# Kernel optimization log

Hardware: AMD Instinct MI355X
Metric: run time of the kernel (lower is better)

The kernel has to match this reference:

```python
import jax, jax.numpy as jnp
import numpy as np

H, KVH, HD, E, TOPK = 16, 4, 128, 8, 2
EPS = 1.1920929e-07  # fp32 machine eps, matches F.rms_norm default


def _rms(v):
    return v * jax.lax.rsqrt(jnp.mean(jnp.square(v), axis=-1, keepdims=True) + EPS)


def _rope(t, cos, sin):
    d = t.shape[-1] // 2
    t1, t2 = t[..., :d], t[..., d:]
    return jnp.concatenate([t1 * cos + t2 * sin, -t1 * sin + t2 * cos], axis=-1)


def setup_inputs():
    key = jax.random.key(0)
    ks = jax.random.split(key, 10)
    B, T, C, D = 2, 1024, 2048, 512
    # real rotary tables (broadcast over batch and heads)
    inv = 1.0 / (10000.0 ** (np.arange(HD // 2, dtype=np.float64) / (HD // 2)))
    ang = np.arange(T, dtype=np.float64)[:, None] * inv[None, :]
    cos = jnp.asarray(np.cos(ang), jnp.float32)[None, :, None, :]
    sin = jnp.asarray(np.sin(ang), jnp.float32)[None, :, None, :]
    w = lambda k, shp, fan: jax.random.normal(k, shp, jnp.float32) * (fan ** -0.5)
    return {
        'x': jax.random.normal(ks[0], (B, T, C), jnp.float32),
        'cos': cos, 'sin': sin,
        'Wq': w(ks[1], (C, C), C),
        'Wk': w(ks[2], (C, KVH * HD), C),
        'Wv': w(ks[3], (C, KVH * HD), C),
        'Wo': w(ks[4], (C, C), C),
        'Wr': w(ks[5], (C, E), C),
        'Ws1': w(ks[6], (C, D), C),
        'Ws2': w(ks[7], (D, C), D),
        'We1': w(ks[8], (E, C, D), C),
        'We2': w(ks[9], (E, D, C), D),
    }


def reference(x, cos, sin, Wq, Wk, Wv, Wo, Wr, Ws1, Ws2, We1, We2):
    B, T, C = x.shape
    # ---- attention (pre-norm, RoPE, QK-norm, GQA, causal SDPA) ----
    xn = _rms(x)
    q = _rms(_rope((xn @ Wq).reshape(B, T, H, HD), cos, sin))      # [B,T,H,HD]
    k = _rms(_rope((xn @ Wk).reshape(B, T, KVH, HD), cos, sin))    # [B,T,KVH,HD]
    v = (xn @ Wv).reshape(B, T, KVH, HD)
    rep = H // KVH
    k = jnp.repeat(k, rep, axis=2)
    v = jnp.repeat(v, rep, axis=2)
    scores = jnp.einsum('bthd,bshd->bhts', q, k) / np.float32(np.sqrt(HD))
    causal = jnp.tril(jnp.ones((T, T), bool))
    scores = jnp.where(causal, scores, jnp.float32(-np.inf))
    att = jax.nn.softmax(scores, axis=-1)
    y = jnp.einsum('bhts,bshd->bthd', att, v).reshape(B, T, C) @ Wo
    x = x + y
    # ---- DeepSeekMoE (shared expert + top-k routed experts) ----
    xf = _rms(x).reshape(-1, C)                                    # [N,C]
    N = xf.shape[0]
    shared = jnp.square(jax.nn.relu(xf @ Ws1)) @ Ws2               # [N,C]
    logits = xf @ Wr                                               # [N,E]
    tk_w, tk_idx = jax.lax.top_k(logits, TOPK)
    tk_w = jax.nn.softmax(tk_w.astype(jnp.float32), axis=-1).astype(x.dtype)
    # scatter top-k probs into dense per-expert gates (indices unique per row)
    gates = jnp.zeros((N, E), x.dtype).at[jnp.arange(N)[:, None], tk_idx].set(tk_w)
    h = jnp.square(jax.nn.relu(jnp.einsum('nc,ecd->end', xf, We1)))  # [E,N,D]
    routed = jnp.einsum('end,edc,ne->nc', h, We2, gates)             # [N,C]
    return x + (shared + routed).reshape(B, T, C)
```

## Files before the change

### kernel.cpp

```cpp
#include <hip/hip_runtime.h>

typedef _Float16 h16;
typedef _Float16 half8 __attribute__((ext_vector_type(8)));
typedef float f32x4 __attribute__((ext_vector_type(4)));

#define EPS_RMS 1.1920929e-07f
#define MiB (1ull << 20)

__device__ __forceinline__ void gload_lds16(const void* g, void* l) {
  __builtin_amdgcn_global_load_lds(
      (const __attribute__((address_space(1))) unsigned int*)g,
      (__attribute__((address_space(3))) unsigned int*)l, 16, 0, 0);
}

struct GemmP {
  const h16* Ah; const h16* Al;
  const h16* Bh; const h16* Bl;
  float* Cf; h16* Ch; h16* Cl;
  const float* R;
  const int* cnt; const int* off; const int* perm;
  long sAz, sBz, sCzHi, sCzLo;
  int M, N, K, lda, ldb, ldc;
  int zAoff, zBoff, zCoff, bzShift, czHiShift, czLoMask;
  float outScale;
};

template <int SPLIT, int EPI, int USECNT, int GATHER, int ASYNC>
__global__ __launch_bounds__(256, 4) void gemm_k(GemmP p) {
  constexpr int NP = SPLIT ? 2 : 1;
  constexpr int NBUF = (ASYNC == 1) ? 2 : 1;
  constexpr int APAD = (ASYNC == 1) ? 32 : 40;
  constexpr int BPAD = (ASYNC >= 1) ? 32 : 40;
  __shared__ __align__(16) h16 As[NBUF][NP][128][APAD];
  __shared__ __align__(16) h16 Bs[NBUF][NP][128][BPAD];
  __shared__ int permLds[GATHER ? 128 : 1];

  int bm, bn, zl;
  if constexpr (USECNT) {
    const int flat2d = blockIdx.y * gridDim.x + blockIdx.x;
    zl = flat2d & 7;
    const int idx = (flat2d >> 3) * 8 + blockIdx.z;
    bm = idx % gridDim.x;
    bn = idx / gridDim.x;
  } else {
    const int nwg = gridDim.x * gridDim.y;
    const int flat = blockIdx.y * gridDim.x + blockIdx.x;
    const int q8 = nwg >> 3, r8 = nwg & 7;
    const int xcd = flat & 7, sub = flat >> 3;
    const int swz = (xcd < r8 ? xcd * (q8 + 1) : r8 * (q8 + 1) + (xcd - r8) * q8) + sub;
    bm = swz % gridDim.x;
    bn = swz / gridDim.x;
    zl = blockIdx.z;
  }

  int Meff, rowbase;
  if (USECNT) {
    Meff = p.cnt[zl]; rowbase = p.off[zl];
    if (bm * 128 >= Meff) return;
  } else { Meff = p.M; rowbase = 0; }

  const int zA = zl + p.zAoff, zB = zl + p.zBoff, zC = zl + p.zCoff;
  const h16* Ah = p.Ah + (size_t)zA * p.sAz;
  const h16* Al = SPLIT ? p.Al + (size_t)zA * p.sAz : (const h16*)0;
  const size_t bofs = (size_t)(zB >> p.bzShift) * p.sBz;
  const h16* Bh = p.Bh + bofs;
  const h16* Bl = SPLIT ? p.Bl + bofs : (const h16*)0;
  const size_t cofs = (size_t)(zC >> p.czHiShift) * p.sCzHi +
                      (size_t)(zC & p.czLoMask) * p.sCzLo;

  const int tid = threadIdx.x;
  const int lane = tid & 63;
  const int wid = tid >> 6, wr = wid >> 1, wc = wid & 1;
  const int fr = lane & 15, fq = lane >> 4;

  if (GATHER) {
    if (tid < 128) {
      const int local = bm * 128 + tid;
      permLds[tid] = (local < Meff) ? p.perm[rowbase + local] : -1;
    }
    __syncthreads();
  }

  const long arow0 = (long)rowbase + (long)bm * 128;

  const f32x4 fz = {0.f, 0.f, 0.f, 0.f};
  f32x4 acc[4][4];
#pragma unroll
  for (int m = 0; m < 4; ++m)
#pragma unroll
    for (int n = 0; n < 4; ++n) acc[m][n] = fz;

  const int nkt = p.K / 32;

  auto compute = [&](int buf) {
    half8 af[NP][4], bf[NP][4];
#pragma unroll
    for (int m = 0; m < 4; ++m) {
      const int r = wr * 64 + m * 16 + fr;
      af[0][m] = *(const half8*)&As[buf][0][r][fq * 8];
      if (SPLIT) af[1][m] = *(const half8*)&As[buf][1][r][fq * 8];
    }
#pragma unroll
    for (int n = 0; n < 4; ++n) {
      const int c = wc * 64 + n * 16 + fr;
      bf[0][n] = *(const half8*)&Bs[buf][0][c][fq * 8];
      if (SPLIT) bf[1][n] = *(const half8*)&Bs[buf][1][c][fq * 8];
    }
#pragma unroll
    for (int m = 0; m < 4; ++m)
#pragma unroll
      for (int n = 0; n < 4; ++n) {
        acc[m][n] = __builtin_amdgcn_mfma_f32_16x16x32_f16(af[0][m], bf[0][n], acc[m][n], 0, 0, 0);
        if (SPLIT) {
          acc[m][n] = __builtin_amdgcn_mfma_f32_16x16x32_f16(af[0][m], bf[1][n], acc[m][n], 0, 0, 0);
          acc[m][n] = __builtin_amdgcn_mfma_f32_16x16x32_f16(af[1][m], bf[0][n], acc[m][n], 0, 0, 0);
        }
      }
  };

  if constexpr (ASYNC == 1) {
    auto stage = [&](int buf, int kt) {
      const int kb = kt * 32;
#pragma unroll
      for (int it = 0; it < 2; ++it) {
        const int d = (tid + it * 256) * 16;
        const int row = d >> 6;
        const int oct = (d >> 4) & 3;
        const size_t gb = ((size_t)(bn * 128 + row)) * p.ldb + kb + oct * 8;
        gload_lds16(Bh + gb, (char*)&Bs[buf][0][0][0] + d);
        if (SPLIT) gload_lds16(Bl + gb, (char*)&Bs[buf][1][0][0] + d);
        const size_t ga = (size_t)(arow0 + row) * p.lda + kb + oct * 8;
        gload_lds16(Ah + ga, (char*)&As[buf][0][0][0] + d);
        if (SPLIT) gload_lds16(Al + ga, (char*)&As[buf][1][0][0] + d);
      }
    };
    stage(0, 0);
    __syncthreads();
    int cur = 0;
    for (int kt = 0; kt < nkt; ++kt) {
      if (kt + 1 < nkt) stage(cur ^ 1, kt + 1);
      compute(cur);
      __syncthreads();
      cur ^= 1;
    }
  } else {
    for (int kt = 0; kt < nkt; ++kt) {
      if (kt) __syncthreads();
      const int kb = kt * 32;
      if constexpr (ASYNC == 2) {
#pragma unroll
        for (int it = 0; it < 2; ++it) {
          const int d = (tid + it * 256) * 16;
          const int row = d >> 6;
          const int oct = (d >> 4) & 3;
          const size_t gb = ((size_t)(bn * 128 + row)) * p.ldb + kb + oct * 8;
          gload_lds16(Bh + gb, (char*)&Bs[0][0][0][0] + d);
          if (SPLIT) gload_lds16(Bl + gb, (char*)&Bs[0][1][0][0] + d);
        }
      }
#pragma unroll
      for (int s = 0; s < 2; ++s) {
        const int seg = tid * 2 + s;
        const int row = seg >> 2, ks = (seg & 3) * 8;
        const int local = bm * 128 + row;
        bool av; long arow;
        if (GATHER) { const int tk2 = permLds[row]; av = (tk2 >= 0); arow = tk2; }
        else { av = (local < Meff); arow = (long)rowbase + local; }
        half8 vh = {0,0,0,0,0,0,0,0}, vl = {0,0,0,0,0,0,0,0};
        if (av) {
          vh = *(const half8*)(Ah + arow * (size_t)p.lda + kb + ks);
          if (SPLIT) vl = *(const half8*)(Al + arow * (size_t)p.lda + kb + ks);
        }
        *(half8*)&As[0][0][row][ks] = vh;
        if (SPLIT) *(half8*)&As[0][1][row][ks] = vl;
        if constexpr (ASYNC == 0) {
          const long brow = (long)bn * 128 + row;
          *(half8*)&Bs[0][0][row][ks] = *(const half8*)(Bh + brow * (size_t)p.ldb + kb + ks);
          if (SPLIT)
            *(half8*)&Bs[0][1][row][ks] = *(const half8*)(Bl + brow * (size_t)p.ldb + kb + ks);
        }
      }
      __syncthreads();
      compute(0);
    }
  }

#pragma unroll
  for (int m = 0; m < 4; ++m)
#pragma unroll
    for (int n = 0; n < 4; ++n)
#pragma unroll
      for (int j = 0; j < 4; ++j) {
        const int rl = wr * 64 + m * 16 + fq * 4 + j;
        const int cl = wc * 64 + n * 16 + fr;
        const int local = bm * 128 + rl;
        if (local >= Meff) continue;
        const size_t idx = cofs + ((size_t)rowbase + local) * p.ldc + (size_t)bn * 128 + cl;
        const float v = acc[m][n][j] * p.outScale;
        if (EPI == 0) p.Cf[idx] = v;
        else if (EPI == 1) p.Cf[idx] = v + p.R[idx];
        else if (EPI == 2) {
          const h16 hh = (h16)v;
          p.Ch[idx] = hh; p.Cl[idx] = (h16)(v - (float)hh);
        } else if (EPI == 3) {
          const float r2 = v > 0.f ? v * v : 0.f;
          p.Ch[idx] = (h16)r2;
        } else {
          p.Ch[idx] = (h16)v;
        }
      }
}

__global__ __launch_bounds__(512, 1) void flash_k(
    const h16* __restrict__ Qh, const h16* __restrict__ Ql,
    const h16* __restrict__ Kh, const h16* __restrict__ Kl,
    const h16* __restrict__ Vh, const h16* __restrict__ Vl,
    h16* __restrict__ yh, h16* __restrict__ yl,
    float* __restrict__ yp, float* __restrict__ mp, float* __restrict__ lp) {
  __shared__ __align__(16) h16 Ks[2][32][136];
  __shared__ __align__(16) h16 Vs[2][128][40];
  __shared__ __align__(16) h16 Ps[8][2][16][40];

  const int item = blockIdx.x, z = blockIdx.y;
  int qb, chunk;
  if (item < 4) { qb = item; chunk = 0; }
  else { qb = 4 + ((item - 4) >> 1); chunk = (item - 4) & 1; }
  const int nt = (qb + 1) * 4;
  const int tBeg = (item < 4) ? 0 : (chunk ? nt / 2 : 0);
  const int tEnd = (item < 4) ? nt : (chunk ? nt : nt / 2);

  const int b = z >> 4, h = z & 15;
  const size_t qoff = (size_t)z * 131072;
  const size_t koff = (size_t)(b * 4 + (h >> 2)) * 131072;

  const int tid = threadIdx.x;
  const int lane = tid & 63, w = tid >> 6;
  const int fr = lane & 15, fq = lane >> 4;

  const int qrow = qb * 128 + w * 16 + fr;
  half8 qa[2][4];
#pragma unroll
  for (int kt = 0; kt < 4; ++kt) {
    qa[0][kt] = *(const half8*)(Qh + qoff + (size_t)qrow * 128 + kt * 32 + fq * 8);
    qa[1][kt] = *(const half8*)(Ql + qoff + (size_t)qrow * 128 + kt * 32 + fq * 8);
  }

  const int kRow = tid >> 4, kSeg = tid & 15;
  const int vRow = tid >> 2, vSeg = tid & 3;

  const f32x4 fz = {0.f, 0.f, 0.f, 0.f};
  f32x4 y[8];
#pragma unroll
  for (int n = 0; n < 8; ++n) y[n] = fz;
  float mrow[4] = {-3.0e38f, -3.0e38f, -3.0e38f, -3.0e38f};
  float lrow[4] = {0.f, 0.f, 0.f, 0.f};

  for (int t = tBeg; t < tEnd; ++t) {
    const int kvb = t * 32;
    if (t != tBeg) __syncthreads();
#pragma unroll
    for (int pl = 0; pl < 2; ++pl) {
      const h16* kp = pl ? Kl : Kh;
      const h16* vp = pl ? Vl : Vh;
      *(half8*)&Ks[pl][kRow][kSeg * 8] =
          *(const half8*)(kp + koff + (size_t)(kvb + kRow) * 128 + kSeg * 8);
      *(half8*)&Vs[pl][vRow][vSeg * 8] =
          *(const half8*)(vp + koff + (size_t)vRow * 1024 + kvb + vSeg * 8);
    }
    __syncthreads();

    f32x4 sf[2] = {fz, fz};
#pragma unroll
    for (int n = 0; n < 2; ++n)
#pragma unroll
      for (int kt = 0; kt < 4; ++kt) {
        const half8 bh2 = *(const half8*)&Ks[0][n * 16 + fr][kt * 32 + fq * 8];
        const half8 bl2 = *(const half8*)&Ks[1][n * 16 + fr][kt * 32 + fq * 8];
        sf[n] = __builtin_amdgcn_mfma_f32_16x16x32_f16(qa[0][kt], bh2, sf[n], 0, 0, 0);
        sf[n] = __builtin_amdgcn_mfma_f32_16x16x32_f16(qa[0][kt], bl2, sf[n], 0, 0, 0);
        sf[n] = __builtin_amdgcn_mfma_f32_16x16x32_f16(qa[1][kt], bh2, sf[n], 0, 0, 0);
      }

    if (kvb + 31 > qb * 128) {
#pragma unroll
      for (int n = 0; n < 2; ++n)
#pragma unroll
        for (int j = 0; j < 4; ++j) {
          const int kvg = kvb + n * 16 + fr;
          const int qg = qb * 128 + w * 16 + fq * 4 + j;
          if (kvg > qg) sf[n][j] = -3.0e38f;
        }
    }

    float al[4];
#pragma unroll
    for (int j = 0; j < 4; ++j) {
      float tm = fmaxf(sf[0][j], sf[1][j]);
#pragma unroll
      for (int msk = 1; msk < 16; msk <<= 1) tm = fmaxf(tm, __shfl_xor(tm, msk, 16));
      const float mn = fmaxf(mrow[j], tm);
      al[j] = __expf(mrow[j] - mn);
      mrow[j] = mn;
      sf[0][j] = __expf(sf[0][j] - mn);
      sf[1][j] = __expf(sf[1][j] - mn);
      float ts = sf[0][j] + sf[1][j];
#pragma unroll
      for (int msk = 1; msk < 16; msk <<= 1) ts += __shfl_xor(ts, msk, 16);
      lrow[j] = lrow[j] * al[j] + ts;
    }
#pragma unroll
    for (int n = 0; n < 8; ++n)
#pragma unroll
      for (int j = 0; j < 4; ++j) y[n][j] *= al[j];

#pragma unroll
    for (int n = 0; n < 2; ++n)
#pragma unroll
      for (int j = 0; j < 4; ++j) {
        const float pp = sf[n][j] * 1024.f;
        const h16 hh = (h16)pp;
        Ps[w][0][fq * 4 + j][n * 16 + fr] = hh;
        Ps[w][1][fq * 4 + j][n * 16 + fr] = (h16)(pp - (float)hh);
      }

    const half8 pah = *(const half8*)&Ps[w][0][fr][fq * 8];
    const half8 pal = *(const half8*)&Ps[w][1][fr][fq * 8];
#pragma unroll
    for (int n = 0; n < 8; ++n) {
      const half8 vh2 = *(const half8*)&Vs[0][n * 16 + fr][fq * 8];
      const half8 vl2 = *(const half8*)&Vs[1][n * 16 + fr][fq * 8];
      y[n] = __builtin_amdgcn_mfma_f32_16x16x32_f16(pah, vh2, y[n], 0, 0, 0);
      y[n] = __builtin_amdgcn_mfma_f32_16x16x32_f16(pah, vl2, y[n], 0, 0, 0);
      y[n] = __builtin_amdgcn_mfma_f32_16x16x32_f16(pal, vh2, y[n], 0, 0, 0);
    }
  }

  if (item < 4) {
#pragma unroll
    for (int n = 0; n < 8; ++n)
#pragma unroll
      for (int j = 0; j < 4; ++j) {
        const int row = qb * 128 + w * 16 + fq * 4 + j;
        const int col = h * 128 + n * 16 + fr;
        const float v = y[n][j] / (1024.f * lrow[j]);
        const size_t idx = ((size_t)(b * 1024 + row)) * 2048 + col;
        const h16 hh = (h16)v;
        yh[idx] = hh; yl[idx] = (h16)(v - (float)hh);
      }
  } else {
#pragma unroll
    for (int j = 0; j < 4; ++j) {
      const int qrl = w * 16 + fq * 4 + j;
      const int q512 = (qb - 4) * 128 + qrl;
      const size_t rbase = (((size_t)chunk * 32 + z) * 512 + q512);
#pragma unroll
      for (int n = 0; n < 8; ++n)
        yp[rbase * 128 + n * 16 + fr] = y[n][j];
      if (fr == 0) { mp[rbase] = mrow[j]; lp[rbase] = lrow[j]; }
    }
  }
}

__global__ void comb_k(const float* __restrict__ yp, const float* __restrict__ mp,
                       const float* __restrict__ lp,
                       h16* __restrict__ yh, h16* __restrict__ yl) {
  const int qh = blockIdx.x, z = blockIdx.y;
  const int b = z >> 4, h = z & 15;
  const int tid = threadIdx.x;
  for (int idx = tid; idx < 16384; idx += 256) {
    const int r = idx >> 7, d = idx & 127;
    const int q512 = qh * 128 + r;
    const size_t r0 = ((size_t)0 * 32 + z) * 512 + q512;
    const size_t r1 = ((size_t)1 * 32 + z) * 512 + q512;
    const float m1 = mp[r0], m2 = mp[r1];
    const float l1 = lp[r0], l2 = lp[r1];
    const float M = fmaxf(m1, m2);
    const float e1 = __expf(m1 - M), e2 = __expf(m2 - M);
    const float inv = 1.f / (1024.f * (l1 * e1 + l2 * e2));
    const float v = (yp[r0 * 128 + d] * e1 + yp[r1 * 128 + d] * e2) * inv;
    const size_t o = ((size_t)(b * 1024 + (4 + qh) * 128 + r)) * 2048 + h * 128 + d;
    const h16 hh = (h16)v;
    yh[o] = hh; yl[o] = (h16)(v - (float)hh);
  }
}

__global__ void tsplit_k(const float* __restrict__ W, h16* __restrict__ Th,
                         h16* __restrict__ Tl, int K, int N, float scale, int wantLo) {
  const size_t eoff = (size_t)blockIdx.z * (size_t)K * N;
  W += eoff; Th += eoff; if (Tl) Tl += eoff;
  __shared__ float tile[32][33];
  const int nt = blockIdx.x * 32, kt = blockIdx.y * 32;
  const int c = threadIdx.x & 31, r0 = threadIdx.x >> 5;
#pragma unroll
  for (int rr = 0; rr < 4; ++rr)
    tile[r0 + rr * 8][c] = W[(size_t)(kt + r0 + rr * 8) * N + nt + c];
  __syncthreads();
#pragma unroll
  for (int rr = 0; rr < 4; ++rr) {
    const int nrow = nt + r0 + rr * 8;
    const float v = tile[c][r0 + rr * 8] * scale;
    const h16 hh = (h16)v;
    Th[(size_t)nrow * K + kt + c] = hh;
    if (wantLo) Tl[(size_t)nrow * K + kt + c] = (h16)(v - (float)hh);
  }
}

template <int WLO, int WSC>
__global__ void rms_k(const float* __restrict__ X, h16* __restrict__ H,
                      h16* __restrict__ L, float* __restrict__ SC) {
  const int row = blockIdx.x;
  const float* x = X + (size_t)row * 2048;
  __shared__ float red[256];
  const int tid = threadIdx.x;
  float ss = 0.f;
  for (int c = tid; c < 2048; c += 256) { const float v = x[c]; ss += v * v; }
  red[tid] = ss; __syncthreads();
  for (int t = 128; t > 0; t >>= 1) {
    if (tid < t) red[tid] += red[tid + t];
    __syncthreads();
  }
  const float sc = rsqrtf(red[0] * (1.f / 2048.f) + EPS_RMS);
  if (WSC && tid == 0) SC[row] = sc;
  for (int c = tid; c < 2048; c += 256) {
    const float v = x[c] * sc;
    const size_t o2 = (size_t)row * 2048 + c;
    const h16 hh = (h16)v;
    H[o2] = hh;
    if (WLO) L[o2] = (h16)(v - (float)hh);
  }
}

__global__ void rope_k(const float* __restrict__ qkv, const float* __restrict__ cosT,
                       const float* __restrict__ sinT,
                       h16* __restrict__ Qh, h16* __restrict__ Ql,
                       h16* __restrict__ Kh, h16* __restrict__ Kl,
                       h16* __restrict__ Vh, h16* __restrict__ Vl) {
  const int tok = blockIdx.x;
  const int b = tok >> 10, t = tok & 1023;
  const int u = blockIdx.y, d = threadIdx.x;
  __shared__ float buf[128];
  __shared__ float red[128];
  int col;
  if (u < 16) col = u * 128 + d;
  else if (u < 20) col = 2048 + (u - 16) * 128 + d;
  else col = 2560 + (u - 20) * 128 + d;
  float v = qkv[(size_t)tok * 3072 + col];
  if (u < 20) {
    buf[d] = v; __syncthreads();
    float r;
    if (d < 64) {
      const float c = cosT[t * 64 + d], s = sinT[t * 64 + d];
      r = buf[d] * c + buf[d + 64] * s;
    } else {
      const float c = cosT[t * 64 + d - 64], s = sinT[t * 64 + d - 64];
      r = -buf[d - 64] * s + buf[d] * c;
    }
    red[d] = r * r; __syncthreads();
    for (int tt = 64; tt > 0; tt >>= 1) {
      if (d < tt) red[d] += red[d + tt];
      __syncthreads();
    }
    v = r * rsqrtf(red[0] * (1.f / 128.f) + EPS_RMS);
    if (u < 16) v *= 0.08838834764831845f;
  }
  const h16 hh = (h16)v;
  const h16 lo = (h16)(v - (float)hh);
  if (u < 16) {
    const size_t o2 = (((size_t)(b * 16 + u)) * 1024 + t) * 128 + d;
    Qh[o2] = hh; Ql[o2] = lo;
  } else if (u < 20) {
    const size_t o2 = (((size_t)(b * 4 + (u - 16))) * 1024 + t) * 128 + d;
    Kh[o2] = hh; Kl[o2] = lo;
  } else {
    const size_t o2 = ((size_t)(b * 4 + (u - 20))) * 131072 + (size_t)d * 1024 + t;
    Vh[o2] = hh; Vl[o2] = lo;
  }
}

__global__ void router_k(const float* __restrict__ x2, const float* __restrict__ rowscale,
                         const float* __restrict__ Wr,
                         int* __restrict__ idx2, float* __restrict__ g2,
                         int* __restrict__ cnt) {
  const int n = blockIdx.x;
  const int tid = threadIdx.x;
  __shared__ float red[256][8];
  float part[8] = {0, 0, 0, 0, 0, 0, 0, 0};
  for (int c = tid; c < 2048; c += 256) {
    const float v = x2[(size_t)n * 2048 + c];
    const float* w2 = Wr + (size_t)c * 8;
#pragma unroll
    for (int e = 0; e < 8; ++e) part[e] += v * w2[e];
  }
#pragma unroll
  for (int e = 0; e < 8; ++e) red[tid][e] = part[e];
  __syncthreads();
  for (int t = 128; t > 0; t >>= 1) {
    if (tid < t)
#pragma unroll
      for (int e = 0; e < 8; ++e) red[tid][e] += red[tid + t][e];
    __syncthreads();
  }
  if (tid == 0) {
    const float sc = rowscale[n];
    float l[8];
#pragma unroll
    for (int e = 0; e < 8; ++e) l[e] = red[0][e] * sc;
    int i1 = 0;
    for (int e = 1; e < 8; ++e) if (l[e] > l[i1]) i1 = e;
    int i2 = (i1 == 0) ? 1 : 0;
    for (int e = 0; e < 8; ++e) if (e != i1 && l[e] > l[i2]) i2 = e;
    const float e2 = __expf(l[i2] - l[i1]);
    const float inv = 1.f / (1.f + e2);
    idx2[n * 2] = i1; idx2[n * 2 + 1] = i2;
    g2[n * 2] = inv; g2[n * 2 + 1] = e2 * inv;
    atomicAdd(&cnt[i1], 1); atomicAdd(&cnt[i2], 1);
  }
}

__global__ void zero8_k(int* __restrict__ p) {
  if (threadIdx.x < 8 && blockIdx.x == 0) p[threadIdx.x] = 0;
}

__global__ void scan_k(const int* __restrict__ cnt, int* __restrict__ off,
                       int* __restrict__ base) {
  if (threadIdx.x == 0 && blockIdx.x == 0) {
    int a = 0;
    for (int e = 0; e < 8; ++e) { off[e] = a; base[e] = a; a += cnt[e]; }
  }
}

__global__ void assign_k(const int* __restrict__ idx2, int* __restrict__ base,
                         int* __restrict__ perm, int* __restrict__ pos2) {
  const int n = blockIdx.x * 256 + threadIdx.x;
  if (n >= 2048) return;
  for (int j = 0; j < 2; ++j) {
    const int e = idx2[n * 2 + j];
    const int pos = atomicAdd(&base[e], 1);
    perm[pos] = n;
    pos2[n * 2 + j] = pos;
  }
}

__global__ void combine_k(const float* __restrict__ x2, const h16* __restrict__ sh,
                          const h16* __restrict__ rp, const int* __restrict__ pos2,
                          const float* __restrict__ g2, float* __restrict__ out) {
  const int n = blockIdx.x;
  const int p0 = pos2[n * 2], p1 = pos2[n * 2 + 1];
  const float g0 = g2[n * 2], g1 = g2[n * 2 + 1];
  for (int c = threadIdx.x; c < 2048; c += 256) {
    const size_t i = (size_t)n * 2048 + c;
    out[i] = x2[i] + (float)sh[i] + g0 * (float)rp[(size_t)p0 * 2048 + c]
             + g1 * (float)rp[(size_t)p1 * 2048 + c];
  }
}

extern "C" void kernel_launch(void* const* d_in, const int* in_sizes, int n_in,
                              void* d_out, int out_size, void* d_ws, size_t ws_size,
                              hipStream_t stream) {
  const float* x    = (const float*)d_in[0];
  const float* cosT = (const float*)d_in[1];
  const float* sinT = (const float*)d_in[2];
  const float* Wq   = (const float*)d_in[3];
  const float* Wk   = (const float*)d_in[4];
  const float* Wv   = (const float*)d_in[5];
  const float* Wo   = (const float*)d_in[6];
  const float* Wr   = (const float*)d_in[7];
  const float* Ws1  = (const float*)d_in[8];
  const float* Ws2  = (const float*)d_in[9];
  const float* We1  = (const float*)d_in[10];
  const float* We2  = (const float*)d_in[11];
  float* out = (float*)d_out;

  unsigned char* W = (unsigned char*)d_ws;
  int*   idx2     = (int*)(W + 0);
  float* g2       = (float*)(W + 16 * 1024);
  int*   cnt      = (int*)(W + 32 * 1024);
  int*   offs     = (int*)(W + 33 * 1024);
  int*   base     = (int*)(W + 34 * 1024);
  int*   perm     = (int*)(W + 36 * 1024);
  int*   pos2     = (int*)(W + 52 * 1024);
  float* rowscale = (float*)(W + 68 * 1024);
  h16* W1h = (h16*)(W + 1 * MiB);
  h16* W1l = (h16*)(W + 13 * MiB);
  h16* W2h = (h16*)(W + 1 * MiB);
  h16* W2l = (h16*)(W + 9 * MiB);
  h16* xnh = (h16*)(W + 25 * MiB);
  h16* xnl = (h16*)(W + 33 * MiB);
  h16* yh  = (h16*)(W + 25 * MiB);
  h16* yl  = (h16*)(W + 33 * MiB);
  h16* xfh = (h16*)(W + 25 * MiB);
  h16* shh = (h16*)(W + 33 * MiB);
  float* qkv = (float*)(W + 41 * MiB);
  float* ypart = (float*)(W + 41 * MiB);
  float* mpart = (float*)(W + 57 * MiB);
  float* lpart = (float*)(W + 58 * MiB);
  h16* hs    = (h16*)(W + 41 * MiB);
  h16* hperm = (h16*)(W + 43 * MiB);
  h16* Qh = (h16*)(W + 65 * MiB);
  h16* Ql = (h16*)(W + 73 * MiB);
  h16* Kh = (h16*)(W + 81 * MiB);
  h16* Kl = (h16*)(W + 83 * MiB);
  h16* Vh = (h16*)(W + 85 * MiB);
  h16* Vl = (h16*)(W + 87 * MiB);
  h16* rph = (h16*)(W + 65 * MiB);
  float* x2 = (float*)(W + 89 * MiB);
  h16* Ws1T = (h16*)(W + 105 * MiB);
  h16* Ws2T = (h16*)(W + 107 * MiB);
  h16* WeT  = (h16*)(W + 109 * MiB);

  const float WS = 64.f;
  const float IWS = 1.f / 64.f;

  tsplit_k<<<dim3(64, 64, 1), 256, 0, stream>>>(Wq, W1h, W1l, 2048, 2048, WS, 1);
  tsplit_k<<<dim3(16, 64, 1), 256, 0, stream>>>(Wk, W1h + (size_t)2048 * 2048,
                                                W1l + (size_t)2048 * 2048, 2048, 512, WS, 1);
  tsplit_k<<<dim3(16, 64, 1), 256, 0, stream>>>(Wv, W1h + (size_t)2560 * 2048,
                                                W1l + (size_t)2560 * 2048, 2048, 512, WS, 1);
  zero8_k<<<1, 64, 0, stream>>>(cnt);
  rms_k<1, 0><<<2048, 256, 0, stream>>>(x, xnh, xnl, (float*)0);
  {
    GemmP p{};
    p.Ah = xnh; p.Al = xnl; p.Bh = W1h; p.Bl = W1l; p.Cf = qkv;
    p.M = 2048; p.N = 3072; p.K = 2048; p.lda = 2048; p.ldb = 2048; p.ldc = 3072;
    p.outScale = IWS;
    gemm_k<1, 0, 0, 0, 1><<<dim3(16, 24, 1), 256, 0, stream>>>(p);
  }

  rope_k<<<dim3(2048, 24, 1), 128, 0, stream>>>(qkv, cosT, sinT, Qh, Ql, Kh, Kl, Vh, Vl);

  tsplit_k<<<dim3(64, 64, 1), 256, 0, stream>>>(Wo, W2h, W2l, 2048, 2048, WS, 1);
  flash_k<<<dim3(12, 32, 1), 512, 0, stream>>>(Qh, Ql, Kh, Kl, Vh, Vl, yh, yl,
                                               ypart, mpart, lpart);
  comb_k<<<dim3(4, 32, 1), 256, 0, stream>>>(ypart, mpart, lpart, yh, yl);

  {
    GemmP p{};
    p.Ah = yh; p.Al = yl; p.Bh = W2h; p.Bl = W2l; p.Cf = x2; p.R = x;
    p.M = 2048; p.N = 2048; p.K = 2048; p.lda = 2048; p.ldb = 2048; p.ldc = 2048;
    p.outScale = IWS;
    gemm_k<1, 1, 0, 0, 1><<<dim3(16, 16, 1), 256, 0, stream>>>(p);
  }

  rms_k<0, 1><<<2048, 256, 0, stream>>>(x2, xfh, (h16*)0, rowscale);
  router_k<<<2048, 256, 0, stream>>>(x2, rowscale, Wr, idx2, g2, cnt);
  scan_k<<<1, 64, 0, stream>>>(cnt, offs, base);
  assign_k<<<8, 256, 0, stream>>>(idx2, base, perm, pos2);

  tsplit_k<<<dim3(16, 64, 1), 256, 0, stream>>>(Ws1, Ws1T, (h16*)0, 2048, 512, WS, 0);
  tsplit_k<<<dim3(64, 16, 1), 256, 0, stream>>>(Ws2, Ws2T, (h16*)0, 512, 2048, WS, 0);
  {
    GemmP p{};
    p.Ah = xfh; p.Bh = Ws1T; p.Ch = hs;
    p.M = 2048; p.N = 512; p.K = 2048; p.lda = 2048; p.ldb = 2048; p.ldc = 512;
    p.outScale = IWS;
    gemm_k<0, 3, 0, 0, 1><<<dim3(16, 4, 1), 256, 0, stream>>>(p);
  }
  {
    GemmP p{};
    p.Ah = hs; p.Bh = Ws2T; p.Ch = shh;
    p.M = 2048; p.N = 2048; p.K = 512; p.lda = 512; p.ldb = 512; p.ldc = 2048;
    p.outScale = IWS;
    gemm_k<0, 4, 0, 0, 1><<<dim3(16, 16, 1), 256, 0, stream>>>(p);
  }
  tsplit_k<<<dim3(16, 64, 8), 256, 0, stream>>>(We1, WeT, (h16*)0, 2048, 512, WS, 0);
  {
    GemmP p{};
    p.Ah = xfh; p.Bh = WeT; p.Ch = hperm;
    p.M = 2048; p.N = 512; p.K = 2048; p.lda = 2048; p.ldb = 2048; p.ldc = 512;
    p.sBz = (long)512 * 2048; p.bzShift = 0;
    p.cnt = cnt; p.off = offs; p.perm = perm;
    p.outScale = IWS;
    gemm_k<0, 3, 1, 1, 2><<<dim3(16, 4, 8), 256, 0, stream>>>(p);
  }
  tsplit_k<<<dim3(64, 16, 8), 256, 0, stream>>>(We2, WeT, (h16*)0, 512, 2048, WS, 0);
  {
    GemmP p{};
    p.Ah = hperm; p.Bh = WeT; p.Cf = (float*)0; p.Ch = rph;
    p.M = 2048; p.N = 2048; p.K = 512; p.lda = 512; p.ldb = 512; p.ldc = 2048;
    p.sBz = (long)2048 * 512; p.bzShift = 0;
    p.cnt = cnt; p.off = offs; p.perm = perm;
    p.outScale = IWS;
    gemm_k<0, 4, 1, 0, 1><<<dim3(16, 16, 8), 256, 0, stream>>>(p);
  }

  combine_k<<<2048, 256, 0, stream>>>(x2, shh, rph, pos2, g2, out);
}
```

Baseline: 598.5 us.

## Prefetch K/V tiles into registers and reorder flash work items longest-first

The flash attention kernel now loads the next K/V tile into registers while the current tile is computed, staging them into LDS at the top of each iteration. Work items are remapped through lookup tables so the longest causal blocks are dispatched first, and the grid is transposed so heads vary fastest. The launch bound is raised to 4 waves-per-EU, which hides global latency and balances the tail but may cap registers and cause spills given the large per-thread accumulator state.

```diff
diff --git a/kernel.cpp b/kernel.cpp
--- a/kernel.cpp
+++ b/kernel.cpp
@@ -211,7 +211,7 @@
       }
 }
 
-__global__ __launch_bounds__(512, 1) void flash_k(
+__global__ __launch_bounds__(512, 4) void flash_k(
     const h16* __restrict__ Qh, const h16* __restrict__ Ql,
     const h16* __restrict__ Kh, const h16* __restrict__ Kl,
     const h16* __restrict__ Vh, const h16* __restrict__ Vl,
@@ -221,13 +221,15 @@
   __shared__ __align__(16) h16 Vs[2][128][40];
   __shared__ __align__(16) h16 Ps[8][2][16][40];
 
-  const int item = blockIdx.x, z = blockIdx.y;
-  int qb, chunk;
-  if (item < 4) { qb = item; chunk = 0; }
-  else { qb = 4 + ((item - 4) >> 1); chunk = (item - 4) & 1; }
+  const int QBT[12]  = {3, 7, 7, 6, 6, 2, 5, 5, 4, 4, 1, 0};
+  const int CHT[12]  = {0, 0, 1, 0, 1, 0, 0, 1, 0, 1, 0, 0};
+  const int FULT[12] = {1, 0, 0, 0, 0, 1, 0, 0, 0, 0, 1, 1};
+
+  const int z = blockIdx.x, item = blockIdx.y;
+  const int qb = QBT[item], chunk = CHT[item], full = FULT[item];
   const int nt = (qb + 1) * 4;
-  const int tBeg = (item < 4) ? 0 : (chunk ? nt / 2 : 0);
-  const int tEnd = (item < 4) ? nt : (chunk ? nt : nt / 2);
+  const int tBeg = full ? 0 : (chunk ? nt / 2 : 0);
+  const int tEnd = full ? nt : (chunk ? nt : nt / 2);
 
   const int b = z >> 4, h = z & 15;
   const size_t qoff = (size_t)z * 131072;
@@ -248,6 +250,18 @@
   const int kRow = tid >> 4, kSeg = tid & 15;
   const int vRow = tid >> 2, vSeg = tid & 3;
 
+  half8 kreg[2], vreg[2];
+  auto loadKV = [&](int t) {
+    const int kvb = t * 32;
+#pragma unroll
+    for (int pl = 0; pl < 2; ++pl) {
+      const h16* kp = pl ? Kl : Kh;
+      const h16* vp = pl ? Vl : Vh;
+      kreg[pl] = *(const half8*)(kp + koff + (size_t)(kvb + kRow) * 128 + kSeg * 8);
+      vreg[pl] = *(const half8*)(vp + koff + (size_t)vRow * 1024 + kvb + vSeg * 8);
+    }
+  };
+
   const f32x4 fz = {0.f, 0.f, 0.f, 0.f};
   f32x4 y[8];
 #pragma unroll
@@ -255,19 +269,17 @@
   float mrow[4] = {-3.0e38f, -3.0e38f, -3.0e38f, -3.0e38f};
   float lrow[4] = {0.f, 0.f, 0.f, 0.f};
 
+  loadKV(tBeg);
   for (int t = tBeg; t < tEnd; ++t) {
     const int kvb = t * 32;
     if (t != tBeg) __syncthreads();
 #pragma unroll
     for (int pl = 0; pl < 2; ++pl) {
-      const h16* kp = pl ? Kl : Kh;
-      const h16* vp = pl ? Vl : Vh;
-      *(half8*)&Ks[pl][kRow][kSeg * 8] =
-          *(const half8*)(kp + koff + (size_t)(kvb + kRow) * 128 + kSeg * 8);
-      *(half8*)&Vs[pl][vRow][vSeg * 8] =
-          *(const half8*)(vp + koff + (size_t)vRow * 1024 + kvb + vSeg * 8);
+      *(half8*)&Ks[pl][kRow][kSeg * 8] = kreg[pl];
+      *(half8*)&Vs[pl][vRow][vSeg * 8] = vreg[pl];
     }
     __syncthreads();
+    if (t + 1 < tEnd) loadKV(t + 1);
 
     f32x4 sf[2] = {fz, fz};
 #pragma unroll
@@ -335,7 +347,7 @@
     }
   }
 
-  if (item < 4) {
+  if (full) {
 #pragma unroll
     for (int n = 0; n < 8; ++n)
 #pragma unroll
@@ -629,7 +641,7 @@
   rope_k<<<dim3(2048, 24, 1), 128, 0, stream>>>(qkv, cosT, sinT, Qh, Ql, Kh, Kl, Vh, Vl);
 
   tsplit_k<<<dim3(64, 64, 1), 256, 0, stream>>>(Wo, W2h, W2l, 2048, 2048, WS, 1);
-  flash_k<<<dim3(12, 32, 1), 512, 0, stream>>>(Qh, Ql, Kh, Kl, Vh, Vl, yh, yl,
+  flash_k<<<dim3(32, 12, 1), 512, 0, stream>>>(Qh, Ql, Kh, Kl, Vh, Vl, yh, yl,
                                                ypart, mpart, lpart);
   comb_k<<<dim3(4, 32, 1), 256, 0, stream>>>(ypart, mpart, lpart, yh, yl);
 
```

Result: no change. 589.6 us (-1.5%).
